# Optimization experiments

Measured on AMD Instinct MI355X. Metric: run time of the kernel, lower is better.

## Reference

```python
import jax, jax.numpy as jnp
import numpy as np

T, D_IN, D_OUT, L, R = 8192, 4096, 4096, 16, 16


def setup_inputs() -> dict:
    key = jax.random.key(0)
    ks = jax.random.split(key, 7)
    x = jax.random.normal(ks[0], (T, D_IN), dtype=jnp.float32)
    W = jax.random.normal(ks[1], (D_OUT, D_IN), dtype=jnp.float32) / np.sqrt(D_IN)
    base_bias = jax.random.normal(ks[2], (D_OUT,), dtype=jnp.float32)
    # stacked LoRA weights (squeezed over the dummy dim-1 in the torch code)
    lora_a = jax.random.normal(ks[3], (L, R, D_IN), dtype=jnp.float32) / np.sqrt(D_IN)
    lora_b = jax.random.normal(ks[4], (L, D_OUT, R), dtype=jnp.float32) / np.sqrt(R)
    bias_stacked = jax.random.normal(ks[5], (L, D_OUT), dtype=jnp.float32)
    # per-token adapter index in [-1, L); -1 means "no LoRA"
    indices = jax.random.randint(ks[6], (T,), -1, L, dtype=jnp.int32)
    return {"x": x, "W": W, "base_bias": base_bias, "lora_a": lora_a,
            "lora_b": lora_b, "bias_stacked": bias_stacked, "indices": indices}


def reference(x, W, base_bias, lora_a, lora_b, bias_stacked, indices):
    num_loras = lora_a.shape[0]
    # base dense GEMM + base bias (ReplicatedLinear.quant_method.apply)
    out = x @ W.T + base_bias  # [T, D_OUT]
    # one_hot gives an all-zero row for indices == -1, matching the masking
    # in apply_bias and the no-op semantics of add_lora for unmapped tokens.
    onehot = jax.nn.one_hot(indices, num_loras, dtype=x.dtype)  # [T, L]
    # per-adapter bias gather-scatter (apply_bias)
    out = out + onehot @ bias_stacked  # [T, D_OUT]
    # SGMV-style LoRA: shrink with A, expand with B, scatter-add into out.
    shrunk_all = jnp.einsum('td,lrd->ltr', x, lora_a)        # [L, T, R]
    shrunk = jnp.einsum('tl,ltr->tr', onehot, shrunk_all)    # [T, R] per-token
    masked = onehot[:, :, None] * shrunk[:, None, :]         # [T, L, R]
    out = out + jnp.einsum('tlr,lor->to', masked, lora_b)    # [T, D_OUT]
    return out
```

## Files before the change

### kernel.cpp

```cpp
#include <hip/hip_runtime.h>
#include <hip/hip_bf16.h>
#include <stdint.h>

typedef unsigned short u16;
typedef unsigned int u32;

#define T_TOK 8192
#define DIN   4096
#define DOUT  4096
#define NL    16
#define NR    16
#define KX    4096
#define K2    4416
#define NKT   68
#define GITERS 34

typedef __attribute__((ext_vector_type(8))) __bf16 bf16x8;
typedef __attribute__((ext_vector_type(4))) float  f32x4;

__device__ __forceinline__ u32 bf16rne(float f) {
    u32 x = __float_as_uint(f);
    return (x + 0x7FFFu + ((x >> 16) & 1u)) >> 16;
}
__device__ __forceinline__ u32 pack2(float a, float b) {
    return bf16rne(a) | (bf16rne(b) << 16);
}

#define NCHUNK_XW ((T_TOK + DOUT) * 512)
#define NCHUNK_BX (DOUT * 32)
#define NCHUNK_LA (NL * NR * DIN / 8)
__global__ void pack_all(const float* __restrict__ x, const float* __restrict__ W,
                         const float* __restrict__ lora_b, const float* __restrict__ la,
                         u16* __restrict__ Abf, u16* __restrict__ Bbf,
                         u16* __restrict__ Aabf) {
    const int total = NCHUNK_XW + NCHUNK_BX + NCHUNK_LA;
    for (int i = blockIdx.x * blockDim.x + threadIdx.x; i < total;
         i += gridDim.x * blockDim.x) {
        const float* s;
        u16* d;
        if (i < NCHUNK_XW) {
            int row = i >> 9;
            int c8  = (i & 511) << 3;
            if (row < T_TOK) { s = x + (size_t)row * DIN + c8; d = Abf + (size_t)row * K2 + c8; }
            else { s = W + (size_t)(row - T_TOK) * DIN + c8; d = Bbf + (size_t)(row - T_TOK) * K2 + c8; }
        } else if (i < NCHUNK_XW + NCHUNK_BX) {
            int j = i - NCHUNK_XW;
            int o = j >> 5;
            int c8 = (j & 31) << 3;
            int l = c8 >> 4, rb = c8 & 15;
            s = lora_b + ((size_t)l * DOUT + o) * NR + rb;
            d = Bbf + (size_t)o * K2 + KX + c8;
        } else {
            int c8 = (i - NCHUNK_XW - NCHUNK_BX) << 3;
            s = la + c8;
            d = Aabf + c8;
        }
        const float4* s4 = (const float4*)s;
        float4 f0 = s4[0], f1 = s4[1];
        uint4 u;
        u.x = pack2(f0.x, f0.y); u.y = pack2(f0.z, f0.w);
        u.z = pack2(f1.x, f1.y); u.w = pack2(f1.z, f1.w);
        *(uint4*)d = u;
    }
}

__global__ __launch_bounds__(256) void zfill_kernel(const u16* __restrict__ Axr,
                                                    const u16* __restrict__ La,
                                                    const int* __restrict__ idx,
                                                    u16* __restrict__ Abf) {
    __shared__ u16 sX[2][64 * 64];
    __shared__ u16 sL[2][64 * 64];
    const int tid  = threadIdx.x;
    const int lane = tid & 63, wid = tid >> 6;
    const int wr = wid >> 1, wc = wid & 1;
    const int lrow = lane & 15;
    const int klo  = (lane >> 4) << 4;
    const int sxr  = (lrow & 7) << 4;
    const int kxb[2] = { klo ^ sxr, (64 + klo) ^ sxr };

    const int bt = blockIdx.x >> 2;
    const int nh = blockIdx.x & 3;

    const int r0 = tid >> 3;
    const int c4 = (tid & 7) ^ (r0 & 7);
    const u16* pX = Axr + (size_t)(bt * 64 + r0) * K2 + c4 * 8;
    const u16* pL = La + (size_t)(nh * 64 + r0) * DIN + c4 * 8;

    f32x4 acc[2][2];
#pragma unroll
    for (int m = 0; m < 2; ++m)
#pragma unroll
        for (int n = 0; n < 2; ++n) { f32x4 z = {0.f,0.f,0.f,0.f}; acc[m][n] = z; }

#define STAGEZ(buf, kt)                                                                 \
  do {                                                                                  \
    __builtin_amdgcn_global_load_lds(                                                   \
      (const __attribute__((address_space(1))) u32*)(pX + (size_t)(kt) * 64),           \
      (__attribute__((address_space(3))) u32*)(&sX[buf][tid * 8]), 16, 0, 0);           \
    __builtin_amdgcn_global_load_lds(                                                   \
      (const __attribute__((address_space(1))) u32*)(pX + (size_t)32 * K2 + (size_t)(kt) * 64),  \
      (__attribute__((address_space(3))) u32*)(&sX[buf][2048 + tid * 8]), 16, 0, 0);    \
    __builtin_amdgcn_global_load_lds(                                                   \
      (const __attribute__((address_space(1))) u32*)(pL + (size_t)(kt) * 64),           \
      (__attribute__((address_space(3))) u32*)(&sL[buf][tid * 8]), 16, 0, 0);           \
    __builtin_amdgcn_global_load_lds(                                                   \
      (const __attribute__((address_space(1))) u32*)(pL + (size_t)32 * DIN + (size_t)(kt) * 64), \
      (__attribute__((address_space(3))) u32*)(&sL[buf][2048 + tid * 8]), 16, 0, 0);    \
  } while (0)

    STAGEZ(0, 0);
    for (int kt = 0; kt < 64; ++kt) {
        const int cur = kt & 1;
        if (kt < 63) {
            STAGEZ(cur ^ 1, kt + 1);
            asm volatile("s_waitcnt vmcnt(4)" ::: "memory");
        } else {
            asm volatile("s_waitcnt vmcnt(0)" ::: "memory");
        }
        __builtin_amdgcn_sched_barrier(0);
        __builtin_amdgcn_s_barrier();
        __builtin_amdgcn_sched_barrier(0);
        const char* sx = (const char*)sX[cur];
        const char* sl = (const char*)sL[cur];
        bf16x8 a[2][2], b[2][2];
#pragma unroll
        for (int m = 0; m < 2; ++m)
#pragma unroll
            for (int kk = 0; kk < 2; ++kk)
                a[m][kk] = *(const bf16x8*)(sx + (wr * 32 + m * 16 + lrow) * 128 + kxb[kk]);
#pragma unroll
        for (int n = 0; n < 2; ++n)
#pragma unroll
            for (int kk = 0; kk < 2; ++kk)
                b[n][kk] = *(const bf16x8*)(sl + (wc * 32 + n * 16 + lrow) * 128 + kxb[kk]);
#pragma unroll
        for (int m = 0; m < 2; ++m)
#pragma unroll
            for (int n = 0; n < 2; ++n)
#pragma unroll
                for (int kk = 0; kk < 2; ++kk)
                    acc[m][n] = __builtin_amdgcn_mfma_f32_16x16x32_bf16(
                        a[m][kk], b[n][kk], acc[m][n], 0, 0, 0);
        __builtin_amdgcn_sched_barrier(0);
        __builtin_amdgcn_s_barrier();
        __builtin_amdgcn_sched_barrier(0);
    }

#pragma unroll
    for (int m = 0; m < 2; ++m) {
#pragma unroll
        for (int rg = 0; rg < 4; ++rg) {
            int t = bt * 64 + wr * 32 + m * 16 + ((lane >> 4) << 2) + rg;
            int l = idx[t];
#pragma unroll
            for (int n = 0; n < 2; ++n) {
                int colr = nh * 64 + wc * 32 + n * 16 + (lane & 15);
                u16 v = ((colr >> 4) == l) ? (u16)bf16rne(acc[m][n][rg]) : (u16)0;
                Abf[(size_t)t * K2 + KX + colr] = v;
            }
        }
    }
}

#define SBAR() __builtin_amdgcn_sched_barrier(0)
#define HWBAR() __builtin_amdgcn_s_barrier()
#define PHASE_BAR() do { SBAR(); HWBAR(); SBAR(); } while (0)
#define VMCNT4() asm volatile("s_waitcnt vmcnt(4)" ::: "memory")
#define VMCNT0() asm volatile("s_waitcnt vmcnt(0)" ::: "memory")

#define STAGE(ptr, h, buf, seg, kt)                                                   \
  do { if ((kt) < NKT) {                                                              \
    __builtin_amdgcn_global_load_lds(                                                 \
      (const __attribute__((address_space(1))) u32*)((ptr) + (size_t)((h)*128 + 0)*K2 + (size_t)(kt)*64),  \
      (__attribute__((address_space(3))) u32*)(lds16 + ((((buf)*4+(seg))<<13) + tid*8)), 16, 0, 0);        \
    __builtin_amdgcn_global_load_lds(                                                 \
      (const __attribute__((address_space(1))) u32*)((ptr) + (size_t)((h)*128 + 64)*K2 + (size_t)(kt)*64), \
      (__attribute__((address_space(3))) u32*)(lds16 + ((((buf)*4+(seg))<<13) + tid*8 + 4096)), 16, 0, 0); \
  } } while (0)

#define RD_AH(buf, mh, aa)                                                            \
  { _Pragma("unroll") for (int mm = 0; mm < 4; ++mm)                                  \
    _Pragma("unroll") for (int kk = 0; kk < 2; ++kk)                                  \
      aa[mm][kk] = *(const bf16x8*)(smem + (((buf)*4 + wr) << 14) + lrow*128          \
          + (mh)*8192 + mm*2048 + kxb[kk]); }

#define RD_BH(buf, nh, bf)                                                            \
  { _Pragma("unroll") for (int nn = 0; nn < 2; ++nn)                                  \
    _Pragma("unroll") for (int kk = 0; kk < 2; ++kk)                                  \
      bf[nn][kk] = *(const bf16x8*)(smem + (((buf)*4 + 2 + (wc>>1)) << 14)            \
          + ((wc&1)*64 + lrow)*128 + ((nh)*2+nn)*2048 + kxb[kk]); }

#define MMQ(mh, nh, aa, bf)                                                           \
  { __builtin_amdgcn_s_setprio(1);                                                    \
    _Pragma("unroll") for (int mm = 0; mm < 4; ++mm)                                  \
    _Pragma("unroll") for (int nn = 0; nn < 2; ++nn)                                  \
    _Pragma("unroll") for (int kk = 0; kk < 2; ++kk)                                  \
      acc[(mh)*4+mm][(nh)*2+nn] = __builtin_amdgcn_mfma_f32_16x16x32_bf16(            \
          aa[mm][kk], bf[nn][kk], acc[(mh)*4+mm][(nh)*2+nn], 0, 0, 0);                \
    __builtin_amdgcn_s_setprio(0); }

__global__ __launch_bounds__(512, 2) void gemm_kernel(const u16* __restrict__ A,
                                                      const u16* __restrict__ B,
                                                      const float* __restrict__ base_bias,
                                                      const float* __restrict__ bias_st,
                                                      const int* __restrict__ gidx,
                                                      float* __restrict__ C) {
    __shared__ u16 lds16[65536];
    const char* smem = (const char*)lds16;

    const int tid  = threadIdx.x;
    const int lane = tid & 63, wid = tid >> 6;
    const int wr = wid >> 2, wc = wid & 3;
    const int lrow = lane & 15;
    const int klo  = (lane >> 4) << 4;
    const int sx   = (lrow & 7) << 4;
    const int kxb[2] = { klo ^ sx, (64 + klo) ^ sx };

    const int wg  = blockIdx.x;
    const int swz = (wg & 7) * 64 + (wg >> 3);
    const int bm = swz >> 4;
    const int bn = swz & 15;

    const int r0  = tid >> 3;
    const int sc4 = (tid & 7) ^ (r0 & 7);
    const u16* pA = A + (size_t)(bm * 256 + r0) * K2 + sc4 * 8;
    const u16* pB = B + (size_t)(bn * 256 + r0) * K2 + sc4 * 8;

    f32x4 acc[8][4];
#pragma unroll
    for (int m = 0; m < 8; ++m)
#pragma unroll
        for (int n = 0; n < 4; ++n) { f32x4 z = {0.f,0.f,0.f,0.f}; acc[m][n] = z; }
    bf16x8 a0[4][2], a1[4][2], bA[2][2], bB[2][2];

    STAGE(pA, 0, 0, 0, 0); STAGE(pA, 1, 0, 1, 0);
    STAGE(pB, 0, 0, 2, 0); STAGE(pB, 1, 0, 3, 0);
    STAGE(pA, 0, 1, 0, 1); STAGE(pB, 0, 1, 2, 1);
    VMCNT4();
    PHASE_BAR();

    for (int i = 0; i < GITERS; ++i) {
        const int kO = 2 * i + 1, kE2 = 2 * i + 2, kO2 = 2 * i + 3;
        RD_AH(0, 0, a0); RD_BH(0, 0, bA); RD_BH(0, 1, bB);
        STAGE(pA, 1, 1, 1, kO); STAGE(pB, 1, 1, 3, kO);
        MMQ(0, 0, a0, bA); MMQ(0, 1, a0, bB);
        PHASE_BAR();
        RD_AH(0, 1, a1);
        STAGE(pA, 0, 0, 0, kE2); STAGE(pB, 0, 0, 2, kE2);
        MMQ(1, 0, a1, bA); MMQ(1, 1, a1, bB);
        if (i == GITERS - 1) { VMCNT0(); } else { VMCNT4(); }
        PHASE_BAR();
        RD_AH(1, 0, a0); RD_BH(1, 0, bA); RD_BH(1, 1, bB);
        STAGE(pA, 1, 0, 1, kE2); STAGE(pB, 1, 0, 3, kE2);
        MMQ(0, 0, a0, bA); MMQ(0, 1, a0, bB);
        PHASE_BAR();
        RD_AH(1, 1, a1);
        STAGE(pA, 0, 1, 0, kO2); STAGE(pB, 0, 1, 2, kO2);
        MMQ(1, 0, a1, bA); MMQ(1, 1, a1, bB);
        VMCNT4();
        PHASE_BAR();
    }

    const int crow0 = bm * 256 + wr * 128 + ((lane >> 4) << 2);
    const int ccol0 = bn * 256 + wc * 64 + (lane & 15);
    float bb[4];
#pragma unroll
    for (int n = 0; n < 4; ++n) bb[n] = base_bias[ccol0 + n * 16];
#pragma unroll
    for (int m = 0; m < 8; ++m) {
#pragma unroll
        for (int rg = 0; rg < 4; ++rg) {
            int row = crow0 + m * 16 + rg;
            int l = gidx[row];
#pragma unroll
            for (int n = 0; n < 4; ++n) {
                float v = acc[m][n][rg] + bb[n];
                if (l >= 0) v += bias_st[(size_t)l * DOUT + ccol0 + n * 16];
                C[(size_t)row * DOUT + ccol0 + n * 16] = v;
            }
        }
    }
}


extern "C" void kernel_launch(void* const* d_in, const int* in_sizes, int n_in,
                              void* d_out, int out_size, void* d_ws, size_t ws_size,
                              hipStream_t stream) {
    const float* x         = (const float*)d_in[0];
    const float* W         = (const float*)d_in[1];
    const float* base_bias = (const float*)d_in[2];
    const float* lora_a    = (const float*)d_in[3];
    const float* lora_b    = (const float*)d_in[4];
    const float* bias_st   = (const float*)d_in[5];
    const int*   indices   = (const int*)d_in[6];
    float* out = (float*)d_out;

    u16* Abf  = (u16*)d_ws;
    u16* Bbf  = Abf + (size_t)T_TOK * K2;
    u16* Aabf = Bbf + (size_t)DOUT * K2;

    pack_all<<<6144, 256, 0, stream>>>(x, W, lora_b, lora_a, Abf, Bbf, Aabf);
    zfill_kernel<<<512, 256, 0, stream>>>(Abf, Aabf, indices, Abf);
    gemm_kernel<<<512, 512, 0, stream>>>(Abf, Bbf, base_bias, bias_st, indices, out);
    (void)in_sizes; (void)n_in; (void)out_size; (void)ws_size;
}
```

Before: 343.3 us.

## Fold base and per-adapter bias into GEMM as an extra one-hot K tile

Appends 64 K-columns to the bf16 operands: A gets a one-hot row (1 for the base bias plus 1 at the token's adapter), and B gets the base bias and the stacked adapter biases converted to bf16. The GEMM runs one extra K-tile after the main loop, and the epilogue becomes a plain store with no bias or index loads. This removes the scattered bias_st and gidx gathers from the epilogue, but the biases are now rounded to bf16, which loses precision, and the MFMA loop gets one more tile of work.

```diff
diff --git a/kernel.cpp b/kernel.cpp
--- a/kernel.cpp
+++ b/kernel.cpp
@@ -12,7 +12,7 @@
 #define NR    16
 #define KX    4096
 #define K2    4416
-#define NKT   68
+#define NKT   69
 #define GITERS 34
 
 typedef __attribute__((ext_vector_type(8))) __bf16 bf16x8;
@@ -27,40 +27,66 @@
 }
 
 #define NCHUNK_XW ((T_TOK + DOUT) * 512)
-#define NCHUNK_BX (DOUT * 32)
+#define NCHUNK_BZ (DOUT * 32)
+#define NCHUNK_BB (DOUT * 8)
 #define NCHUNK_LA (NL * NR * DIN / 8)
 __global__ void pack_all(const float* __restrict__ x, const float* __restrict__ W,
-                         const float* __restrict__ lora_b, const float* __restrict__ la,
+                         const float* __restrict__ lora_b,
+                         const float* __restrict__ base_bias,
+                         const float* __restrict__ bias_st,
+                         const float* __restrict__ la,
                          u16* __restrict__ Abf, u16* __restrict__ Bbf,
                          u16* __restrict__ Aabf) {
-    const int total = NCHUNK_XW + NCHUNK_BX + NCHUNK_LA;
+    const int total = NCHUNK_XW + NCHUNK_BZ + NCHUNK_BB + NCHUNK_LA;
     for (int i = blockIdx.x * blockDim.x + threadIdx.x; i < total;
          i += gridDim.x * blockDim.x) {
-        const float* s;
-        u16* d;
-        if (i < NCHUNK_XW) {
-            int row = i >> 9;
-            int c8  = (i & 511) << 3;
-            if (row < T_TOK) { s = x + (size_t)row * DIN + c8; d = Abf + (size_t)row * K2 + c8; }
-            else { s = W + (size_t)(row - T_TOK) * DIN + c8; d = Bbf + (size_t)(row - T_TOK) * K2 + c8; }
-        } else if (i < NCHUNK_XW + NCHUNK_BX) {
-            int j = i - NCHUNK_XW;
-            int o = j >> 5;
-            int c8 = (j & 31) << 3;
-            int l = c8 >> 4, rb = c8 & 15;
-            s = lora_b + ((size_t)l * DOUT + o) * NR + rb;
-            d = Bbf + (size_t)o * K2 + KX + c8;
+        if (i < NCHUNK_XW + NCHUNK_BZ) {
+            const float* s;
+            u16* d;
+            if (i < NCHUNK_XW) {
+                int row = i >> 9;
+                int c8  = (i & 511) << 3;
+                if (row < T_TOK) { s = x + (size_t)row * DIN + c8; d = Abf + (size_t)row * K2 + c8; }
+                else { s = W + (size_t)(row - T_TOK) * DIN + c8; d = Bbf + (size_t)(row - T_TOK) * K2 + c8; }
+            } else {
+                int j = i - NCHUNK_XW;
+                int o = j >> 5;
+                int c8 = (j & 31) << 3;
+                int l = c8 >> 4, rb = c8 & 15;
+                s = lora_b + ((size_t)l * DOUT + o) * NR + rb;
+                d = Bbf + (size_t)o * K2 + KX + c8;
+            }
+            const float4* s4 = (const float4*)s;
+            float4 f0 = s4[0], f1 = s4[1];
+            uint4 u;
+            u.x = pack2(f0.x, f0.y); u.y = pack2(f0.z, f0.w);
+            u.z = pack2(f1.x, f1.y); u.w = pack2(f1.z, f1.w);
+            *(uint4*)d = u;
+        } else if (i < NCHUNK_XW + NCHUNK_BZ + NCHUNK_BB) {
+            int j = i - NCHUNK_XW - NCHUNK_BZ;
+            int o = j >> 3;
+            int c8 = (j & 7) << 3;
+            u32 w[4];
+#pragma unroll
+            for (int q = 0; q < 4; ++q) {
+                float v0 = 0.f, v1 = 0.f;
+                int e0 = c8 + 2 * q;
+                if (e0 == 0) v0 = base_bias[o];
+                else if (e0 <= 16) v0 = bias_st[(size_t)(e0 - 1) * DOUT + o];
+                int e1 = e0 + 1;
+                if (e1 <= 16) v1 = bias_st[(size_t)(e1 - 1) * DOUT + o];
+                w[q] = pack2(v0, v1);
+            }
+            *(uint4*)(Bbf + (size_t)o * K2 + KX + 256 + c8) = *(uint4*)w;
         } else {
-            int c8 = (i - NCHUNK_XW - NCHUNK_BX) << 3;
-            s = la + c8;
-            d = Aabf + c8;
+            int c8 = (i - NCHUNK_XW - NCHUNK_BZ - NCHUNK_BB) << 3;
+            const float4* s4 = (const float4*)(la + c8);
+            float4 f0 = s4[0], f1 = s4[1];
+            uint4 u;
+            u.x = pack2(f0.x, f0.y); u.y = pack2(f0.z, f0.w);
+            u.z = pack2(f1.x, f1.y); u.w = pack2(f1.z, f1.w);
+            *(uint4*)(Aabf + c8) = u;
         }
-        const float4* s4 = (const float4*)s;
-        float4 f0 = s4[0], f1 = s4[1];
-        uint4 u;
-        u.x = pack2(f0.x, f0.y); u.y = pack2(f0.z, f0.w);
-        u.z = pack2(f1.x, f1.y); u.w = pack2(f1.z, f1.w);
-        *(uint4*)d = u;
     }
 }
 
@@ -160,6 +186,24 @@
             }
         }
     }
+    if (nh == 0) {
+        int tl = tid >> 2;
+        int q4 = tid & 3;
+        int t = bt * 64 + tl;
+        int l = idx[t];
+        u32 w[8];
+#pragma unroll
+        for (int q = 0; q < 8; ++q) {
+            int e0 = q4 * 16 + 2 * q;
+            u32 v0 = (e0 == 0 || (l >= 0 && e0 == 1 + l)) ? 0x3F80u : 0u;
+            int e1 = e0 + 1;
+            u32 v1 = (e1 == 0 || (l >= 0 && e1 == 1 + l)) ? 0x3F80u : 0u;
+            w[q] = v0 | (v1 << 16);
+        }
+        u16* dst = Abf + (size_t)t * K2 + KX + 256 + q4 * 16;
+        *(uint4*)dst = *(uint4*)&w[0];
+        *(uint4*)(dst + 8) = *(uint4*)&w[4];
+    }
 }
 
 #define SBAR() __builtin_amdgcn_sched_barrier(0)
@@ -201,9 +245,6 @@
 
 __global__ __launch_bounds__(512, 2) void gemm_kernel(const u16* __restrict__ A,
                                                       const u16* __restrict__ B,
-                                                      const float* __restrict__ base_bias,
-                                                      const float* __restrict__ bias_st,
-                                                      const int* __restrict__ gidx,
                                                       float* __restrict__ C) {
     __shared__ u16 lds16[65536];
     const char* smem = (const char*)lds16;
@@ -248,7 +289,7 @@
         RD_AH(0, 1, a1);
         STAGE(pA, 0, 0, 0, kE2); STAGE(pB, 0, 0, 2, kE2);
         MMQ(1, 0, a1, bA); MMQ(1, 1, a1, bB);
-        if (i == GITERS - 1) { VMCNT0(); } else { VMCNT4(); }
+        VMCNT4();
         PHASE_BAR();
         RD_AH(1, 0, a0); RD_BH(1, 0, bA); RD_BH(1, 1, bB);
         STAGE(pA, 1, 0, 1, kE2); STAGE(pB, 1, 0, 3, kE2);
@@ -261,25 +302,20 @@
         PHASE_BAR();
     }
 
+    VMCNT0();
+    PHASE_BAR();
+    RD_AH(0, 0, a0); RD_AH(0, 1, a1); RD_BH(0, 0, bA); RD_BH(0, 1, bB);
+    MMQ(0, 0, a0, bA); MMQ(1, 0, a1, bA); MMQ(0, 1, a0, bB); MMQ(1, 1, a1, bB);
+
     const int crow0 = bm * 256 + wr * 128 + ((lane >> 4) << 2);
     const int ccol0 = bn * 256 + wc * 64 + (lane & 15);
-    float bb[4];
-#pragma unroll
-    for (int n = 0; n < 4; ++n) bb[n] = base_bias[ccol0 + n * 16];
-#pragma unroll
-    for (int m = 0; m < 8; ++m) {
-#pragma unroll
-        for (int rg = 0; rg < 4; ++rg) {
-            int row = crow0 + m * 16 + rg;
-            int l = gidx[row];
-#pragma unroll
-            for (int n = 0; n < 4; ++n) {
-                float v = acc[m][n][rg] + bb[n];
-                if (l >= 0) v += bias_st[(size_t)l * DOUT + ccol0 + n * 16];
-                C[(size_t)row * DOUT + ccol0 + n * 16] = v;
-            }
-        }
-    }
+#pragma unroll
+    for (int m = 0; m < 8; ++m)
+#pragma unroll
+        for (int n = 0; n < 4; ++n)
+#pragma unroll
+            for (int rg = 0; rg < 4; ++rg)
+                C[(size_t)(crow0 + m * 16 + rg) * DOUT + ccol0 + n * 16] = acc[m][n][rg];
 }
 
 
@@ -299,8 +335,9 @@
     u16* Bbf  = Abf + (size_t)T_TOK * K2;
     u16* Aabf = Bbf + (size_t)DOUT * K2;
 
-    pack_all<<<6144, 256, 0, stream>>>(x, W, lora_b, lora_a, Abf, Bbf, Aabf);
+    pack_all<<<6144, 256, 0, stream>>>(x, W, lora_b, base_bias, bias_st, lora_a,
+                                       Abf, Bbf, Aabf);
     zfill_kernel<<<512, 256, 0, stream>>>(Abf, Aabf, indices, Abf);
-    gemm_kernel<<<512, 512, 0, stream>>>(Abf, Bbf, base_bias, bias_st, indices, out);
+    gemm_kernel<<<512, 512, 0, stream>>>(Abf, Bbf, out);
     (void)in_sizes; (void)n_in; (void)out_size; (void)ws_size;
 }
```

Result: faster. 326.7 us, median of 2 (-4.8%).
